# Performance work log

Measured on AMD Instinct MI355X. Metric: run time of the kernel, lower is better.

## Reference

```python
import jax, jax.numpy as jnp
import numpy as np

B, H, S, D = 2, 16, 2048, 128

def setup_inputs() -> dict:
    key = jax.random.key(0)
    kq, kk, kv = jax.random.split(key, 3)
    q = jax.random.normal(kq, (B, H, S, D), dtype=jnp.float32)
    k = jax.random.normal(kk, (B, H, S, D), dtype=jnp.float32)
    v = jax.random.normal(kv, (B, H, S, D), dtype=jnp.float32)
    # causal mask, broadcastable over batch and heads; 0 -> masked out
    mask = jnp.tril(jnp.ones((S, S), dtype=jnp.int32))[None, None, :, :]
    return {"q": q, "k": k, "v": v, "mask": mask}

def reference(q, k, v, mask):
    # scores: [B,H,S,S] -- note: module applies NO 1/sqrt(d) scaling
    attn = jnp.einsum('bhqd,bhkd->bhqk', q, k)
    neg_inf = jnp.finfo(attn.dtype).min
    attn = jnp.where(mask == 0, neg_inf, attn)
    attn = jax.nn.softmax(attn, axis=-1)
    out = jnp.einsum('bhqk,bhkd->bhqd', attn, v)
    return out
```

## Files before the change

### kernel.cpp

```cpp
#include <hip/hip_runtime.h>


#define SQ 2048
#define DH 128
#define BM 64
#define BN 64
#define NELEM 8388608

typedef _Float16 f16x8 __attribute__((ext_vector_type(8)));
typedef float f32x4 __attribute__((ext_vector_type(4)));
typedef unsigned short u16x8 __attribute__((ext_vector_type(8)));

typedef __attribute__((address_space(3))) void lds_t;
typedef __attribute__((address_space(1))) void gmem_t;

__device__ __forceinline__ void gload16(void* lds, const void* g) {
  __builtin_amdgcn_global_load_lds((const gmem_t*)g, (lds_t*)lds, 16, 0, 0);
}

__device__ __forceinline__ unsigned short f2h(float f) {
  return __builtin_bit_cast(unsigned short, (_Float16)f);
}

__global__ __launch_bounds__(256) void prep(const float* __restrict__ k,
                                            const float* __restrict__ v,
                                            unsigned short* __restrict__ ko,
                                            unsigned short* __restrict__ vt) {
  const int tid = threadIdx.x;
  const int bx = blockIdx.x;
  if (bx < 1024) {
    __shared__ unsigned short lv[64 * 132];
    const int bh = bx >> 5;
    const int s0 = (bx & 31) * 64;
    const float* vs = v + ((size_t)bh * SQ + s0) * DH;
    #pragma unroll
    for (int it = 0; it < 8; ++it) {
      int fi = it * 256 + tid;
      int sL = fi >> 5;
      int dL = (fi & 31) * 4;
      float4 val = *(const float4*)(vs + (size_t)sL * DH + dL);
      ushort4 o;
      o.x = f2h(val.x); o.y = f2h(val.y); o.z = f2h(val.z); o.w = f2h(val.w);
      *(ushort4*)(lv + sL * 132 + dL) = o;
    }
    __syncthreads();
    #pragma unroll
    for (int it = 0; it < 4; ++it) {
      int ci = it * 256 + tid;
      int dL = ci >> 3;
      int sg = ci & 7;
      u16x8 o;
      #pragma unroll
      for (int j = 0; j < 8; ++j) o[j] = lv[(sg * 8 + j) * 132 + dL];
      *(u16x8*)(vt + ((size_t)bh * DH + dL) * SQ + s0 + sg * 8) = o;
    }
  } else {
    const int NT = NELEM / 4;
    for (int i = (bx - 1024) * 256 + tid; i < NT; i += 2048 * 256) {
      float4 val = ((const float4*)k)[i];
      ushort4 o;
      o.x = f2h(val.x); o.y = f2h(val.y); o.z = f2h(val.z); o.w = f2h(val.w);
      ((ushort4*)ko)[i] = o;
    }
  }
}

__global__ __launch_bounds__(256, 4) void fattn(const float* __restrict__ Qf,
                                                const unsigned short* __restrict__ Kh,
                                                const unsigned short* __restrict__ Vth,
                                                float* __restrict__ Out) {
  __shared__ char smem[40960];
  const int tid  = threadIdx.x;
  const int wave = tid >> 6;
  const int lane = tid & 63;
  const int quad = lane >> 4;
  const int c    = lane & 15;

  const int t     = (int)blockIdx.x;
  const int xcd   = t & 7;
  const int idx   = t >> 3;
  const int cu    = idx & 31;
  const int round = idx >> 5;
  const int bh    = xcd * 4 + round;
  int qb;
  {
    int b0 = (cu + 8 * (round >> 1)) & 31;
    qb = (round & 1) ? (31 - b0) : b0;
  }
  const int rowbase = qb * BM;

  char* sK = smem;
  char* sV = smem + 16384;
  char* sP = smem + 32768 + wave * 2048;

  const float* Qg = Qf + ((size_t)bh * SQ + rowbase) * DH;
  #pragma unroll
  for (int it = 0; it < 8; ++it) {
    int gi  = it * 256 + tid;
    int row = gi >> 5;
    int sub = gi & 31;
    float4 qv = *(const float4*)(Qg + (size_t)row * DH + sub * 4);
    ushort4 h;
    h.x = f2h(qv.x); h.y = f2h(qv.y); h.z = f2h(qv.z); h.w = f2h(qv.w);
    int gr = (sub >> 1) ^ (row & 7);
    *(ushort4*)(smem + row * 256 + gr * 16 + (sub & 1) * 8) = h;
  }
  __syncthreads();
  f16x8 qf[4];
  {
    int rl = wave * 16 + c;
    #pragma unroll
    for (int ch = 0; ch < 4; ++ch) {
      int gr = (ch * 4 + quad) ^ (c & 7);
      qf[ch] = *(const f16x8*)(smem + rl * 256 + gr * 16);
    }
  }
  __syncthreads();

  f32x4 acc[8];
  #pragma unroll
  for (int dt = 0; dt < 8; ++dt) acc[dt] = (f32x4){0.f, 0.f, 0.f, 0.f};
  float mo = -1e30f, lrow = 0.f;

  const unsigned short* Kbase = Kh + (size_t)bh * SQ * DH;
  const unsigned short* Vbase = Vth + (size_t)bh * DH * SQ;
  const int nkt = qb + 1;

  for (int kt = 0; kt < nkt; ++kt) {
    const int k0 = kt * BN;
    #pragma unroll
    for (int it = 0; it < 4; ++it) {
      int gi  = it * 256 + tid;
      int key = gi >> 4;
      int dg  = (gi & 15) ^ (key & 7);
      gload16(sK + (it * 256 + wave * 64) * 16,
              Kbase + (size_t)(k0 + key) * DH + dg * 8);
    }
    #pragma unroll
    for (int it = 0; it < 4; ++it) {
      int gi = it * 256 + tid;
      int d  = gi >> 3;
      int kg = (gi & 7) ^ (d & 7);
      gload16(sV + (it * 256 + wave * 64) * 16,
              Vbase + (size_t)d * SQ + k0 + kg * 8);
    }
    __syncthreads();

    const bool diag  = (kt == qb);
    const int ntmax  = diag ? wave : 3;
    const int chmax  = diag ? (wave >> 1) : 1;

    f32x4 sc[4];
    #pragma unroll
    for (int nt = 0; nt < 4; ++nt) sc[nt] = (f32x4){0.f, 0.f, 0.f, 0.f};
    #pragma unroll
    for (int nt = 0; nt < 4; ++nt) {
      if (nt <= ntmax) {
        int keyl = nt * 16 + c;
        #pragma unroll
        for (int ch = 0; ch < 4; ++ch) {
          int gr = (ch * 4 + quad) ^ (c & 7);
          f16x8 kf = *(const f16x8*)(sK + keyl * 256 + gr * 16);
          sc[nt] = __builtin_amdgcn_mfma_f32_16x16x32_f16(kf, qf[ch], sc[nt], 0, 0, 0);
        }
      }
    }

    if (diag) {
      int rl = wave * 16 + c;
      #pragma unroll
      for (int nt = 0; nt < 4; ++nt)
        #pragma unroll
        for (int r = 0; r < 4; ++r)
          if (nt * 16 + quad * 4 + r > rl) sc[nt][r] = -1e30f;
    }

    float cm = -1e30f;
    #pragma unroll
    for (int nt = 0; nt < 4; ++nt)
      #pragma unroll
      for (int r = 0; r < 4; ++r) cm = fmaxf(cm, sc[nt][r]);
    cm = fmaxf(cm, __shfl_xor(cm, 16));
    cm = fmaxf(cm, __shfl_xor(cm, 32));
    float mn = fmaxf(mo, cm);
    float al = __expf(mo - mn);
    float rs = 0.f;
    ushort4 pk[4];
    #pragma unroll
    for (int nt = 0; nt < 4; ++nt) {
      #pragma unroll
      for (int r = 0; r < 4; ++r) {
        float p = __expf(sc[nt][r] - mn);
        rs += p;
        ((unsigned short*)&pk[nt])[r] = f2h(p);
      }
    }
    rs += __shfl_xor(rs, 16);
    rs += __shfl_xor(rs, 32);
    lrow = lrow * al + rs;
    mo = mn;
    #pragma unroll
    for (int dt = 0; dt < 8; ++dt) acc[dt] *= al;

    #pragma unroll
    for (int nt = 0; nt < 4; ++nt) {
      int g8 = nt * 2 + (quad >> 1);
      *(ushort4*)(sP + c * 128 + ((g8 ^ (c & 7)) * 16) + (quad & 1) * 8) = pk[nt];
    }

    #pragma unroll
    for (int ch = 0; ch < 2; ++ch) {
      if (ch <= chmax) {
        f16x8 pf = *(const f16x8*)(sP + c * 128 + (((ch * 4 + quad) ^ (c & 7)) * 16));
        #pragma unroll
        for (int dt = 0; dt < 8; ++dt) {
          int d  = dt * 16 + c;
          int gr = (ch * 4 + quad) ^ (c & 7);
          f16x8 vf = *(const f16x8*)(sV + d * 128 + gr * 16);
          acc[dt] = __builtin_amdgcn_mfma_f32_16x16x32_f16(vf, pf, acc[dt], 0, 0, 0);
        }
      }
    }
    __syncthreads();
  }

  const float inv = 1.0f / lrow;
  const int rowg = rowbase + wave * 16 + c;
  float* op = Out + ((size_t)bh * SQ + rowg) * DH;
  #pragma unroll
  for (int dt = 0; dt < 8; ++dt) {
    float4 o;
    o.x = acc[dt][0] * inv;
    o.y = acc[dt][1] * inv;
    o.z = acc[dt][2] * inv;
    o.w = acc[dt][3] * inv;
    *(float4*)(op + dt * 16 + quad * 4) = o;
  }
}

extern "C" void kernel_launch(void* const* d_in, const int* in_sizes, int n_in,
                              void* d_out, int out_size, void* d_ws, size_t ws_size,
                              hipStream_t stream) {
  const float* q = (const float*)d_in[0];
  const float* k = (const float*)d_in[1];
  const float* v = (const float*)d_in[2];
  float* out = (float*)d_out;

  unsigned short* kws = (unsigned short*)d_ws;
  unsigned short* vws = kws + NELEM;

  prep<<<3072, 256, 0, stream>>>(k, v, kws, vws);
  fattn<<<1024, 256, 0, stream>>>(q, kws, vws, out);
}
```

Baseline: 216.9 us.

## Use two-wave blocks with two query row tiles per wave and exp2 softmax

```diff
diff --git a/kernel.cpp b/kernel.cpp
--- a/kernel.cpp
+++ b/kernel.cpp
@@ -6,6 +6,7 @@
 #define BM 64
 #define BN 64
 #define NELEM 8388608
+#define LOG2E 1.44269504088896340736f
 
 typedef _Float16 f16x8 __attribute__((ext_vector_type(8)));
 typedef float f32x4 __attribute__((ext_vector_type(4)));
@@ -17,10 +18,10 @@
 __device__ __forceinline__ void gload16(void* lds, const void* g) {
   __builtin_amdgcn_global_load_lds((const gmem_t*)g, (lds_t*)lds, 16, 0, 0);
 }
-
 __device__ __forceinline__ unsigned short f2h(float f) {
   return __builtin_bit_cast(unsigned short, (_Float16)f);
 }
+__device__ __forceinline__ int xor3(int row) { return (row ^ (row >> 3)) & 7; }
 
 __global__ __launch_bounds__(256) void prep(const float* __restrict__ k,
                                             const float* __restrict__ v,
@@ -28,13 +29,13 @@
                                             unsigned short* __restrict__ vt) {
   const int tid = threadIdx.x;
   const int bx = blockIdx.x;
-  if (bx < 1024) {
-    __shared__ unsigned short lv[64 * 132];
-    const int bh = bx >> 5;
-    const int s0 = (bx & 31) * 64;
+  if (bx < 2048) {
+    __shared__ unsigned short lv[32 * 132];
+    const int bh = bx >> 6;
+    const int s0 = (bx & 63) * 32;
     const float* vs = v + ((size_t)bh * SQ + s0) * DH;
     #pragma unroll
-    for (int it = 0; it < 8; ++it) {
+    for (int it = 0; it < 4; ++it) {
       int fi = it * 256 + tid;
       int sL = fi >> 5;
       int dL = (fi & 31) * 4;
@@ -45,10 +46,10 @@
     }
     __syncthreads();
     #pragma unroll
-    for (int it = 0; it < 4; ++it) {
+    for (int it = 0; it < 2; ++it) {
       int ci = it * 256 + tid;
-      int dL = ci >> 3;
-      int sg = ci & 7;
+      int dL = ci >> 2;
+      int sg = ci & 3;
       u16x8 o;
       #pragma unroll
       for (int j = 0; j < 8; ++j) o[j] = lv[(sg * 8 + j) * 132 + dL];
@@ -56,7 +57,7 @@
     }
   } else {
     const int NT = NELEM / 4;
-    for (int i = (bx - 1024) * 256 + tid; i < NT; i += 2048 * 256) {
+    for (int i = (bx - 2048) * 256 + tid; i < NT; i += 2048 * 256) {
       float4 val = ((const float4*)k)[i];
       ushort4 o;
       o.x = f2h(val.x); o.y = f2h(val.y); o.z = f2h(val.z); o.w = f2h(val.w);
@@ -65,7 +66,7 @@
   }
 }
 
-__global__ __launch_bounds__(256, 4) void fattn(const float* __restrict__ Qf,
+__global__ __launch_bounds__(128, 2) void fattn(const float* __restrict__ Qf,
                                                 const unsigned short* __restrict__ Kh,
                                                 const unsigned short* __restrict__ Vth,
                                                 float* __restrict__ Out) {
@@ -91,36 +92,43 @@
 
   char* sK = smem;
   char* sV = smem + 16384;
-  char* sP = smem + 32768 + wave * 2048;
+  char* sP = smem + 32768 + wave * 4096;
+
+  const int rb0 = wave * 16;
+  const int rb1 = 32 + wave * 16;
 
   const float* Qg = Qf + ((size_t)bh * SQ + rowbase) * DH;
   #pragma unroll
-  for (int it = 0; it < 8; ++it) {
-    int gi  = it * 256 + tid;
+  for (int it = 0; it < 16; ++it) {
+    int gi  = it * 128 + tid;
     int row = gi >> 5;
     int sub = gi & 31;
     float4 qv = *(const float4*)(Qg + (size_t)row * DH + sub * 4);
     ushort4 h;
-    h.x = f2h(qv.x); h.y = f2h(qv.y); h.z = f2h(qv.z); h.w = f2h(qv.w);
-    int gr = (sub >> 1) ^ (row & 7);
+    h.x = f2h(qv.x * LOG2E); h.y = f2h(qv.y * LOG2E);
+    h.z = f2h(qv.z * LOG2E); h.w = f2h(qv.w * LOG2E);
+    int gr = (sub >> 1) ^ xor3(row);
     *(ushort4*)(smem + row * 256 + gr * 16 + (sub & 1) * 8) = h;
   }
   __syncthreads();
-  f16x8 qf[4];
-  {
-    int rl = wave * 16 + c;
+  f16x8 qf[2][4];
+  #pragma unroll
+  for (int mt = 0; mt < 2; ++mt) {
+    int row = (mt ? rb1 : rb0) + c;
     #pragma unroll
     for (int ch = 0; ch < 4; ++ch) {
-      int gr = (ch * 4 + quad) ^ (c & 7);
-      qf[ch] = *(const f16x8*)(smem + rl * 256 + gr * 16);
+      int gr = (ch * 4 + quad) ^ xor3(row);
+      qf[mt][ch] = *(const f16x8*)(smem + row * 256 + gr * 16);
     }
   }
   __syncthreads();
 
-  f32x4 acc[8];
-  #pragma unroll
-  for (int dt = 0; dt < 8; ++dt) acc[dt] = (f32x4){0.f, 0.f, 0.f, 0.f};
-  float mo = -1e30f, lrow = 0.f;
+  f32x4 acc[2][8];
+  #pragma unroll
+  for (int mt = 0; mt < 2; ++mt)
+    #pragma unroll
+    for (int dt = 0; dt < 8; ++dt) acc[mt][dt] = (f32x4){0.f, 0.f, 0.f, 0.f};
+  float mo[2] = {-1e30f, -1e30f}, lrow[2] = {0.f, 0.f};
 
   const unsigned short* Kbase = Kh + (size_t)bh * SQ * DH;
   const unsigned short* Vbase = Vth + (size_t)bh * DH * SQ;
@@ -129,112 +137,135 @@
   for (int kt = 0; kt < nkt; ++kt) {
     const int k0 = kt * BN;
     #pragma unroll
-    for (int it = 0; it < 4; ++it) {
-      int gi  = it * 256 + tid;
+    for (int it = 0; it < 8; ++it) {
+      int gi  = it * 128 + tid;
       int key = gi >> 4;
-      int dg  = (gi & 15) ^ (key & 7);
-      gload16(sK + (it * 256 + wave * 64) * 16,
+      int dg  = (gi & 15) ^ xor3(key);
+      gload16(sK + (it * 128 + wave * 64) * 16,
               Kbase + (size_t)(k0 + key) * DH + dg * 8);
     }
     #pragma unroll
-    for (int it = 0; it < 4; ++it) {
-      int gi = it * 256 + tid;
+    for (int it = 0; it < 8; ++it) {
+      int gi = it * 128 + tid;
       int d  = gi >> 3;
-      int kg = (gi & 7) ^ (d & 7);
-      gload16(sV + (it * 256 + wave * 64) * 16,
+      int kg = (gi & 7) ^ xor3(d);
+      gload16(sV + (it * 128 + wave * 64) * 16,
               Vbase + (size_t)d * SQ + k0 + kg * 8);
     }
     __syncthreads();
 
-    const bool diag  = (kt == qb);
-    const int ntmax  = diag ? wave : 3;
-    const int chmax  = diag ? (wave >> 1) : 1;
-
-    f32x4 sc[4];
-    #pragma unroll
-    for (int nt = 0; nt < 4; ++nt) sc[nt] = (f32x4){0.f, 0.f, 0.f, 0.f};
+    const bool diag = (kt == qb);
+    const int ntm0 = diag ? wave : 3;
+    const int ntm1 = diag ? 2 + wave : 3;
+
+    f32x4 sc[2][4];
+    #pragma unroll
+    for (int mt = 0; mt < 2; ++mt)
+      #pragma unroll
+      for (int nt = 0; nt < 4; ++nt) sc[mt][nt] = (f32x4){0.f, 0.f, 0.f, 0.f};
     #pragma unroll
     for (int nt = 0; nt < 4; ++nt) {
-      if (nt <= ntmax) {
-        int keyl = nt * 16 + c;
+      int keyl = nt * 16 + c;
+      int xr = xor3(keyl);
+      bool do0 = (nt <= ntm0);
+      bool do1 = (nt <= ntm1);
+      #pragma unroll
+      for (int ch = 0; ch < 4; ++ch) {
+        f16x8 kf = *(const f16x8*)(sK + keyl * 256 + (((ch * 4 + quad) ^ xr) * 16));
+        if (do0) sc[0][nt] = __builtin_amdgcn_mfma_f32_16x16x32_f16(kf, qf[0][ch], sc[0][nt], 0, 0, 0);
+        if (do1) sc[1][nt] = __builtin_amdgcn_mfma_f32_16x16x32_f16(kf, qf[1][ch], sc[1][nt], 0, 0, 0);
+      }
+    }
+
+    if (diag) {
+      #pragma unroll
+      for (int mt = 0; mt < 2; ++mt) {
+        int rl  = (mt ? rb1 : rb0) + c;
+        int ntm = mt ? ntm1 : ntm0;
         #pragma unroll
-        for (int ch = 0; ch < 4; ++ch) {
-          int gr = (ch * 4 + quad) ^ (c & 7);
-          f16x8 kf = *(const f16x8*)(sK + keyl * 256 + gr * 16);
-          sc[nt] = __builtin_amdgcn_mfma_f32_16x16x32_f16(kf, qf[ch], sc[nt], 0, 0, 0);
-        }
-      }
-    }
-
-    if (diag) {
-      int rl = wave * 16 + c;
+        for (int nt = 0; nt < 4; ++nt)
+          #pragma unroll
+          for (int r = 0; r < 4; ++r) {
+            int key = nt * 16 + quad * 4 + r;
+            if (nt > ntm || (nt == ntm && key > rl)) sc[mt][nt][r] = -1e30f;
+          }
+      }
+    }
+
+    #pragma unroll
+    for (int mt = 0; mt < 2; ++mt) {
+      float cm = -1e30f;
       #pragma unroll
       for (int nt = 0; nt < 4; ++nt)
         #pragma unroll
-        for (int r = 0; r < 4; ++r)
-          if (nt * 16 + quad * 4 + r > rl) sc[nt][r] = -1e30f;
-    }
-
-    float cm = -1e30f;
-    #pragma unroll
-    for (int nt = 0; nt < 4; ++nt)
-      #pragma unroll
-      for (int r = 0; r < 4; ++r) cm = fmaxf(cm, sc[nt][r]);
-    cm = fmaxf(cm, __shfl_xor(cm, 16));
-    cm = fmaxf(cm, __shfl_xor(cm, 32));
-    float mn = fmaxf(mo, cm);
-    float al = __expf(mo - mn);
-    float rs = 0.f;
-    ushort4 pk[4];
-    #pragma unroll
-    for (int nt = 0; nt < 4; ++nt) {
-      #pragma unroll
-      for (int r = 0; r < 4; ++r) {
-        float p = __expf(sc[nt][r] - mn);
-        rs += p;
-        ((unsigned short*)&pk[nt])[r] = f2h(p);
-      }
-    }
-    rs += __shfl_xor(rs, 16);
-    rs += __shfl_xor(rs, 32);
-    lrow = lrow * al + rs;
-    mo = mn;
-    #pragma unroll
-    for (int dt = 0; dt < 8; ++dt) acc[dt] *= al;
-
-    #pragma unroll
-    for (int nt = 0; nt < 4; ++nt) {
-      int g8 = nt * 2 + (quad >> 1);
-      *(ushort4*)(sP + c * 128 + ((g8 ^ (c & 7)) * 16) + (quad & 1) * 8) = pk[nt];
-    }
-
+        for (int r = 0; r < 4; ++r) cm = fmaxf(cm, sc[mt][nt][r]);
+      cm = fmaxf(cm, __shfl_xor(cm, 16));
+      cm = fmaxf(cm, __shfl_xor(cm, 32));
+      float mn = fmaxf(mo[mt], cm);
+      float al = exp2f(mo[mt] - mn);
+      float rs = 0.f;
+      ushort4 pk[4];
+      #pragma unroll
+      for (int nt = 0; nt < 4; ++nt)
+        #pragma unroll
+        for (int r = 0; r < 4; ++r) {
+          float p = exp2f(sc[mt][nt][r] - mn);
+          rs += p;
+          ((unsigned short*)&pk[nt])[r] = f2h(p);
+        }
+      rs += __shfl_xor(rs, 16);
+      rs += __shfl_xor(rs, 32);
+      lrow[mt] = lrow[mt] * al + rs;
+      mo[mt] = mn;
+      #pragma unroll
+      for (int dt = 0; dt < 8; ++dt) acc[mt][dt] *= al;
+      int rp = mt * 16 + c;
+      int xr = xor3(rp);
+      #pragma unroll
+      for (int nt = 0; nt < 4; ++nt) {
+        int g8 = nt * 2 + (quad >> 1);
+        *(ushort4*)(sP + rp * 128 + ((g8 ^ xr) * 16) + (quad & 1) * 8) = pk[nt];
+      }
+    }
+
+    const bool pv0full = !diag;
     #pragma unroll
     for (int ch = 0; ch < 2; ++ch) {
-      if (ch <= chmax) {
-        f16x8 pf = *(const f16x8*)(sP + c * 128 + (((ch * 4 + quad) ^ (c & 7)) * 16));
-        #pragma unroll
-        for (int dt = 0; dt < 8; ++dt) {
-          int d  = dt * 16 + c;
-          int gr = (ch * 4 + quad) ^ (c & 7);
-          f16x8 vf = *(const f16x8*)(sV + d * 128 + gr * 16);
-          acc[dt] = __builtin_amdgcn_mfma_f32_16x16x32_f16(vf, pf, acc[dt], 0, 0, 0);
-        }
+      bool d0 = (ch == 0) | pv0full;
+      f16x8 pf0, pf1;
+      {
+        int rp = c;  int xr = xor3(rp);
+        if (d0) pf0 = *(const f16x8*)(sP + rp * 128 + (((ch * 4 + quad) ^ xr) * 16));
+      }
+      {
+        int rp = 16 + c;  int xr = xor3(rp);
+        pf1 = *(const f16x8*)(sP + rp * 128 + (((ch * 4 + quad) ^ xr) * 16));
+      }
+      #pragma unroll
+      for (int dt = 0; dt < 8; ++dt) {
+        int d = dt * 16 + c;
+        f16x8 vf = *(const f16x8*)(sV + d * 128 + (((ch * 4 + quad) ^ xor3(d)) * 16));
+        if (d0) acc[0][dt] = __builtin_amdgcn_mfma_f32_16x16x32_f16(vf, pf0, acc[0][dt], 0, 0, 0);
+        acc[1][dt] = __builtin_amdgcn_mfma_f32_16x16x32_f16(vf, pf1, acc[1][dt], 0, 0, 0);
       }
     }
     __syncthreads();
   }
 
-  const float inv = 1.0f / lrow;
-  const int rowg = rowbase + wave * 16 + c;
-  float* op = Out + ((size_t)bh * SQ + rowg) * DH;
-  #pragma unroll
-  for (int dt = 0; dt < 8; ++dt) {
-    float4 o;
-    o.x = acc[dt][0] * inv;
-    o.y = acc[dt][1] * inv;
-    o.z = acc[dt][2] * inv;
-    o.w = acc[dt][3] * inv;
-    *(float4*)(op + dt * 16 + quad * 4) = o;
+  #pragma unroll
+  for (int mt = 0; mt < 2; ++mt) {
+    const float inv = 1.0f / lrow[mt];
+    const int rowg = rowbase + (mt ? rb1 : rb0) + c;
+    float* op = Out + ((size_t)bh * SQ + rowg) * DH;
+    #pragma unroll
+    for (int dt = 0; dt < 8; ++dt) {
+      float4 o;
+      o.x = acc[mt][dt][0] * inv;
+      o.y = acc[mt][dt][1] * inv;
+      o.z = acc[mt][dt][2] * inv;
+      o.w = acc[mt][dt][3] * inv;
+      *(float4*)(op + dt * 16 + quad * 4) = o;
+    }
   }
 }
 
@@ -249,6 +280,6 @@
   unsigned short* kws = (unsigned short*)d_ws;
   unsigned short* vws = kws + NELEM;
 
-  prep<<<3072, 256, 0, stream>>>(k, v, kws, vws);
-  fattn<<<1024, 256, 0, stream>>>(q, kws, vws, out);
-}
+  prep<<<4096, 256, 0, stream>>>(k, v, kws, vws);
+  fattn<<<1024, 128, 0, stream>>>(q, kws, vws, out);
+}
```

Result: slower. 241.0 us (+11.1%).
